# Performance work log

Measured on AMD Instinct MI355X. Metric: run time of the kernel, lower is better.

Reference implementation:

```python
import jax, jax.numpy as jnp
import numpy as np

N, S, D = 512, 64, 128   # num_nodes, seq_len, model_size
H, K = 4, 32             # num_heads, key_size
E = 4096                 # num_edges
WF = 4                   # widening_factor
EPS = 1e-5


def _alibi(num_heads, seq_len):
    slopes = 2.0 ** (-8.0 * (jnp.arange(1, num_heads + 1, dtype=jnp.float32) / num_heads))
    pos = jnp.arange(seq_len, dtype=jnp.float32)
    rel = pos[None, :] - pos[:, None]  # T - t, <= 0 in causal region
    return (slopes[:, None, None] * rel)[None]  # [1,H,S,S]


def layer_norm(x, scale, offset):
    mu = jnp.mean(x, axis=-1, keepdims=True)
    var = jnp.var(x, axis=-1, keepdims=True)
    return (x - mu) * jax.lax.rsqrt(var + EPS) * scale + offset


def segment_softmax(logits, seg, num_segments):
    maxs = jax.ops.segment_max(logits, seg, num_segments=num_segments)
    e = jnp.exp(logits - maxs[seg])
    denom = jax.ops.segment_sum(e, seg, num_segments=num_segments)
    return e / denom[seg]


def setup_inputs() -> dict:
    key = jax.random.key(0)
    ks = jax.random.split(key, 24)
    sd = 0.02
    inp = {
        'nodes': jax.random.normal(ks[0], (N, S, D), jnp.float32),
        'senders': jax.random.randint(ks[1], (E,), 0, N, jnp.int32),
        'receivers': jax.random.randint(ks[2], (E,), 0, N, jnp.int32),
        'alibi_mask': _alibi(H, S),
        'ln1_s': jnp.ones((D,)), 'ln1_b': jnp.zeros((D,)),
        'wq': jax.random.normal(ks[3], (D, H * K)) * sd, 'bq': jnp.zeros((H * K,)),
        'wk': jax.random.normal(ks[4], (D, H * K)) * sd, 'bk': jnp.zeros((H * K,)),
        'wv': jax.random.normal(ks[5], (D, H * K)) * sd, 'bv': jnp.zeros((H * K,)),
        'wo': jax.random.normal(ks[6], (H * K, D)) * sd, 'bo': jnp.zeros((D,)),
        'ln2_s': jnp.ones((D,)), 'ln2_b': jnp.zeros((D,)),
        'w1': jax.random.normal(ks[7], (D, WF * D)) * sd, 'b1': jnp.zeros((WF * D,)),
        'w2': jax.random.normal(ks[8], (WF * D, D)) * sd, 'b2': jnp.zeros((D,)),
        'ln3_s': jnp.ones((D,)), 'ln3_b': jnp.zeros((D,)),
        'w_sa': jax.random.normal(ks[9], (2 * D, D)) * sd, 'b_sa': jnp.zeros((D,)),
        'w_sq': jax.random.normal(ks[10], (D, H * D)) * sd, 'b_sq': jnp.zeros((H * D,)),
    }
    return inp


def reference(nodes, senders, receivers, alibi_mask,
              ln1_s, ln1_b, wq, bq, wk, bk, wv, bv, wo, bo,
              ln2_s, ln2_b, w1, b1, w2, b2, ln3_s, ln3_b,
              w_sa, b_sa, w_sq, b_sq):
    n, s, d = nodes.shape
    # --- node self-attention with ALiBi + causal mask ---
    xn = layer_norm(nodes, ln1_s, ln1_b)
    q = (xn @ wq + bq).reshape(n, s, H, K)
    k = (xn @ wk + bk).reshape(n, s, H, K)
    v = (xn @ wv + bv).reshape(n, s, H, K)
    logits = jnp.einsum('nthk,nThk->nhtT', q, k)
    logits = alibi_mask + logits / jnp.sqrt(jnp.float32(K))
    causal = jnp.tril(jnp.ones((1, 1, s, s), dtype=bool))
    logits = jnp.where(causal, logits, -1e30)
    w = jax.nn.softmax(logits, axis=-1)
    attn = jnp.einsum('nhtT,nThk->nthk', w, v).reshape(n, s, H * K)
    nodes = nodes + (attn @ wo + bo)  # dropout rate 0 (eval)
    # --- FFN block ---
    xn = layer_norm(nodes, ln2_s, ln2_b)
    dense = jax.nn.gelu(xn @ w1 + b1) @ w2 + b2
    nodes = layer_norm(nodes + dense, ln3_s, ln3_b)
    # --- graph message passing: gather / segment-softmax / segment-sum ---
    sent = nodes[senders]        # [E,S,D]
    recv = nodes[receivers]      # [E,S,D]
    sl = jnp.concatenate([sent, recv], axis=-1) @ w_sa + b_sa  # [E,S,D]
    aw = segment_softmax(sl, receivers, n)                     # [E,S,D]
    sq = (aw @ w_sq + b_sq).reshape(E, s, H, d)                # [E,S,H,D]
    messages = jnp.mean(sq * sent[:, :, None, :], axis=2)      # [E,S,D]
    out = jax.ops.segment_sum(messages, receivers, num_segments=n)
    return out
```

## Files before the change

### kernel.cpp

```cpp
#include <hip/hip_runtime.h>
#include <hip/hip_bf16.h>

typedef __hip_bfloat16 bf16;
typedef __attribute__((ext_vector_type(8))) __bf16 bf8v;
typedef __attribute__((ext_vector_type(4))) float  f4v;

#define NN 512
#define SSEQ 64
#define DDIM 128
#define HH 4
#define NROWS (NN*SSEQ)
#define EMAX 4096
#define ECH 64

__device__ __forceinline__ float b2f(bf16 x){ return __bfloat162float(x); }
__device__ __forceinline__ bf16 f2b(float x){ return __float2bfloat16(x); }
__device__ __forceinline__ float ldf(float x){ return x; }
__device__ __forceinline__ float ldf(bf16 x){ return b2f(x); }
__device__ __forceinline__ void stf(float* p, float v){ *p = v; }
__device__ __forceinline__ void stf(bf16* p, float v){ *p = f2b(v); }

__device__ __forceinline__ f4v mfma16(bf8v a, bf8v b, f4v c){
  return __builtin_amdgcn_mfma_f32_16x16x32_bf16(a, b, c, 0, 0, 0);
}
__device__ __forceinline__ bf8v ldfrag(const void* p){
  return __builtin_bit_cast(bf8v, *(const int4*)p);
}

__global__ __launch_bounds__(256) void prep_all_k(
    const float* wq, const float* wk, const float* wv, const float* wo,
    const float* w1, const float* w2, const float* wsa,
    const float* w_sq, const float* b_sq,
    const float* bq, const float* bk, const float* bv,
    bf16* wqkvT, bf16* woT, bf16* w1T, bf16* w2T, bf16* wsaTt,
    bf16* wbarT, float* bbar, float* qkv_bias){
  int b = blockIdx.x, t = threadIdx.x;
  if (b < 832){
    const float* W; bf16* Wt; int K, lN, rel, roff = 0;
    if      (b < 64) { W=wq;  Wt=wqkvT; K=128; lN=7; rel=b;     roff=0;   }
    else if (b <128) { W=wk;  Wt=wqkvT; K=128; lN=7; rel=b-64;  roff=128; }
    else if (b <192) { W=wv;  Wt=wqkvT; K=128; lN=7; rel=b-128; roff=256; }
    else if (b <256) { W=wo;  Wt=woT;   K=128; lN=7; rel=b-192; }
    else if (b <512) { W=w1;  Wt=w1T;   K=128; lN=9; rel=b-256; }
    else if (b <768) { W=w2;  Wt=w2T;   K=512; lN=7; rel=b-512; }
    else             { W=wsa; Wt=wsaTt; K=128; lN=7; rel=b-768; }
    int i = rel*256 + t;
    int k = i >> lN, n = i & ((1<<lN)-1);
    Wt[(size_t)(n+roff)*K + k] = f2b(W[i]);
  } else if (b < 896){
    int i = (b-832)*256 + t;
    int c = i>>7, d = i&127;
    float s = 0.f;
    #pragma unroll
    for (int h=0;h<HH;++h) s += w_sq[(size_t)c*(HH*DDIM) + h*DDIM + d];
    wbarT[d*DDIM + c] = f2b(0.25f*s);
  } else {
    int idx = (b-896)*256 + t;
    if (idx < 128){
      float s = 0.f;
      #pragma unroll
      for (int h=0;h<HH;++h) s += b_sq[h*DDIM + idx];
      bbar[idx] = 0.25f*s;
    } else if (idx < 512){
      int j = idx - 128;
      float v = (j<128) ? bq[j] : (j<256) ? bk[j-128] : bv[j-256];
      qkv_bias[j] = v;
    }
  }
}

__global__ __launch_bounds__(512) void csr_off_k(const int* __restrict__ receivers,
    int* __restrict__ off, int* __restrict__ perm, int E){
  __shared__ int s_cnt[NN];
  int t = threadIdx.x;
  s_cnt[t] = 0;
  __syncthreads();
  for (int e=t; e<E; e+=512) atomicAdd(&s_cnt[receivers[e]], 1);
  __syncthreads();
  int deg = s_cnt[t];
  int acc = 0, myrank = 0;
  for (int i=0;i<NN;++i){
    int di = s_cnt[i];
    acc    += (i<t) ? di : 0;
    myrank += ((di > deg) || (di == deg && i < t)) ? 1 : 0;
  }
  off[t] = acc;
  if (t==NN-1) off[NN] = acc + deg;
  perm[myrank] = t;
}

__global__ __launch_bounds__(64) void hist_k(const int* __restrict__ receivers,
    int* __restrict__ chunk_cnt, int E){
  __shared__ int hc[NN];
  int t = threadIdx.x, c = blockIdx.x;
  for (int i=t;i<NN;i+=64) hc[i]=0;
  __syncthreads();
  int e = c*ECH + t;
  if (e < E) atomicAdd(&hc[receivers[e]], 1);
  __syncthreads();
  for (int i=t;i<NN;i+=64) chunk_cnt[(size_t)c*NN + i] = hc[i];
}

__global__ __launch_bounds__(512) void base_k(const int* __restrict__ off,
    const int* __restrict__ chunk_cnt, int* __restrict__ base, int nch){
  int n = threadIdx.x;
  int run = off[n];
  for (int c=0;c<nch;++c){
    base[(size_t)c*NN + n] = run;
    run += chunk_cnt[(size_t)c*NN + n];
  }
}

__global__ __launch_bounds__(64) void slot_k(const int* __restrict__ senders,
    const int* __restrict__ receivers, const int* __restrict__ base,
    int* __restrict__ slot_snd, int E){
  int t = threadIdx.x, c = blockIdx.x;
  int e = c*ECH + t;
  bool valid = (e < E);
  int r  = valid ? receivers[e] : -1;
  int sd = valid ? senders[e]   : 0;
  int rank = 0;
  #pragma unroll
  for (int i=0;i<64;++i){
    int ri = __shfl(r, i);
    rank += (i < t && ri == r) ? 1 : 0;
  }
  if (valid) slot_snd[base[(size_t)c*NN + r] + rank] = sd;
}

template<typename TIN, typename TOUT>
__global__ __launch_bounds__(256) void ln_k(const TIN* __restrict__ x,
    const float* __restrict__ sc, const float* __restrict__ of,
    TOUT* __restrict__ y){
  int row  = blockIdx.x*4 + (threadIdx.x>>6);
  int lane = threadIdx.x & 63;
  size_t base = (size_t)row*DDIM;
  float v0 = ldf(x[base+lane]);
  float v1 = ldf(x[base+lane+64]);
  float s = v0+v1, q = v0*v0+v1*v1;
  #pragma unroll
  for (int m=1;m<64;m<<=1){ s += __shfl_xor(s,m); q += __shfl_xor(q,m); }
  float mu   = s*(1.0f/DDIM);
  float var  = q*(1.0f/DDIM) - mu*mu;
  float rstd = rsqrtf(var + 1e-5f);
  stf(&y[base+lane],    (v0-mu)*rstd*sc[lane]    + of[lane]);
  stf(&y[base+lane+64], (v1-mu)*rstd*sc[lane+64] + of[lane+64]);
}

template<int KT, int ACT, typename TR, bool RES, bool BIAS>
__global__ __launch_bounds__(256) void gemm_m(const bf16* __restrict__ A,
    const bf16* __restrict__ Wt, const float* __restrict__ bias,
    const TR* __restrict__ R, bf16* __restrict__ C, int N){
  __shared__ bf16 sA[64][72];
  __shared__ bf16 sB[64][72];
  int t = threadIdx.x;
  int bm = blockIdx.x, bn = blockIdx.y;
  int w = t>>6, lane = t&63;
  int wr = w>>1, wc = w&1;
  f4v acc[2][2] = {};
  for (int ks=0; ks<KT; ks+=64){
    #pragma unroll
    for (int p=0;p<2;++p){
      int r = p*32 + (t>>3), cc = (t&7)*8;
      *(int4*)(&sA[r][cc]) = *(const int4*)(A  + (size_t)(bm*64+r)*KT + ks + cc);
      *(int4*)(&sB[r][cc]) = *(const int4*)(Wt + (size_t)(bn*64+r)*KT + ks + cc);
    }
    __syncthreads();
    #pragma unroll
    for (int k0=0;k0<64;k0+=32){
      int kc = k0 + 8*(lane>>4);
      bf8v a0 = ldfrag(&sA[wr*32      + (lane&15)][kc]);
      bf8v a1 = ldfrag(&sA[wr*32 + 16 + (lane&15)][kc]);
      bf8v b0 = ldfrag(&sB[wc*32      + (lane&15)][kc]);
      bf8v b1 = ldfrag(&sB[wc*32 + 16 + (lane&15)][kc]);
      acc[0][0] = mfma16(a0, b0, acc[0][0]);
      acc[0][1] = mfma16(a0, b1, acc[0][1]);
      acc[1][0] = mfma16(a1, b0, acc[1][0]);
      acc[1][1] = mfma16(a1, b1, acc[1][1]);
    }
    __syncthreads();
  }
  #pragma unroll
  for (int j=0;j<2;++j){
    int gcol = bn*64 + wc*32 + j*16 + (lane&15);
    float bs = BIAS ? bias[gcol] : 0.f;
    #pragma unroll
    for (int i=0;i<2;++i){
      #pragma unroll
      for (int r=0;r<4;++r){
        int grow = bm*64 + wr*32 + i*16 + 4*(lane>>4) + r;
        float v = acc[i][j][r] + bs;
        if (ACT==1){
          float xx = v;
          v = 0.5f*xx*(1.0f + tanhf(0.7978845608028654f*(xx + 0.044715f*xx*xx*xx)));
        }
        if (ACT==2) v = __expf(v);
        if (RES) v += ldf(R[(size_t)grow*N + gcol]);
        C[(size_t)grow*N + gcol] = f2b(v);
      }
    }
  }
}

__global__ __launch_bounds__(256) void gemm_wo_ln2_k(const bf16* __restrict__ A,
    const bf16* __restrict__ Wt, const float* __restrict__ bias,
    const float* __restrict__ Rres, const float* __restrict__ lns,
    const float* __restrict__ lnb, bf16* __restrict__ n2out,
    bf16* __restrict__ xnout){
  __shared__ bf16 sA[64][72];
  __shared__ bf16 sB[128][72];
  __shared__ float s_st[2][2][32][2];
  int t = threadIdx.x, bm = blockIdx.x;
  int w = t>>6, lane = t&63, ls = lane&15, lg = lane>>4;
  int wr = w>>1, wc = w&1;
  f4v acc[2][4] = {};
  for (int ks=0; ks<128; ks+=64){
    #pragma unroll
    for (int p=0;p<2;++p){
      int r = p*32 + (t>>3), cc = (t&7)*8;
      *(int4*)(&sA[r][cc]) = *(const int4*)(A + (size_t)(bm*64+r)*128 + ks + cc);
    }
    #pragma unroll
    for (int p=0;p<4;++p){
      int r = p*32 + (t>>3), cc = (t&7)*8;
      *(int4*)(&sB[r][cc]) = *(const int4*)(Wt + (size_t)r*128 + ks + cc);
    }
    __syncthreads();
    #pragma unroll
    for (int k0=0;k0<64;k0+=32){
      int kc = k0 + 8*lg;
      bf8v a0 = ldfrag(&sA[wr*32      + ls][kc]);
      bf8v a1 = ldfrag(&sA[wr*32 + 16 + ls][kc]);
      #pragma unroll
      for (int j=0;j<4;++j){
        bf8v bj = ldfrag(&sB[wc*64 + j*16 + ls][kc]);
        acc[0][j] = mfma16(a0, bj, acc[0][j]);
        acc[1][j] = mfma16(a1, bj, acc[1][j]);
      }
    }
    __syncthreads();
  }
  float x[2][4][4];
  float psum[2][4], psq[2][4];
  #pragma unroll
  for (int i=0;i<2;++i)
    #pragma unroll
    for (int r=0;r<4;++r){ psum[i][r]=0.f; psq[i][r]=0.f; }
  #pragma unroll
  for (int i=0;i<2;++i){
    #pragma unroll
    for (int j=0;j<4;++j){
      int col = wc*64 + j*16 + ls;
      float bs = bias[col];
      #pragma unroll
      for (int r=0;r<4;++r){
        int row = bm*64 + wr*32 + i*16 + 4*lg + r;
        float v = acc[i][j][r] + bs + Rres[(size_t)row*128 + col];
        x[i][j][r] = v;
        psum[i][r] += v;
        psq[i][r]  += v*v;
        n2out[(size_t)row*128 + col] = f2b(v);
      }
    }
  }
  #pragma unroll
  for (int i=0;i<2;++i)
    #pragma unroll
    for (int r=0;r<4;++r){
      float s_=psum[i][r], q_=psq[i][r];
      s_ += __shfl_xor(s_,1); s_ += __shfl_xor(s_,2);
      s_ += __shfl_xor(s_,4); s_ += __shfl_xor(s_,8);
      q_ += __shfl_xor(q_,1); q_ += __shfl_xor(q_,2);
      q_ += __shfl_xor(q_,4); q_ += __shfl_xor(q_,8);
      if (ls == 0){
        int rl = i*16 + 4*lg + r;
        s_st[wr][wc][rl][0] = s_;
        s_st[wr][wc][rl][1] = q_;
      }
    }
  __syncthreads();
  #pragma unroll
  for (int i=0;i<2;++i){
    #pragma unroll
    for (int r=0;r<4;++r){
      int rl = i*16 + 4*lg + r;
      float s_ = s_st[wr][0][rl][0] + s_st[wr][1][rl][0];
      float q_ = s_st[wr][0][rl][1] + s_st[wr][1][rl][1];
      float mu = s_*(1.0f/DDIM);
      float var = q_*(1.0f/DDIM) - mu*mu;
      float rstd = rsqrtf(var + 1e-5f);
      int row = bm*64 + wr*32 + rl;
      #pragma unroll
      for (int j=0;j<4;++j){
        int col = wc*64 + j*16 + ls;
        xnout[(size_t)row*128 + col] = f2b((x[i][j][r]-mu)*rstd*lns[col] + lnb[col]);
      }
    }
  }
}

__global__ __launch_bounds__(256) void gemm_w2_tail_k(const bf16* __restrict__ A,
    const bf16* __restrict__ Wt, const float* __restrict__ bias,
    const bf16* __restrict__ Rres, const float* __restrict__ lns,
    const float* __restrict__ lnb, const bf16* __restrict__ wsaT,
    bf16* __restrict__ r2out, bf16* __restrict__ yexpout){
  __shared__ bf16 sA[64][72];
  __shared__ bf16 sB[128][72];
  __shared__ bf16 sY[64][136];
  __shared__ float s_st[2][2][32][2];
  int t = threadIdx.x, bm = blockIdx.x;
  int w = t>>6, lane = t&63, ls = lane&15, lg = lane>>4;
  int wr = w>>1, wc = w&1;
  f4v acc[2][4] = {};
  for (int ks=0; ks<512; ks+=64){
    #pragma unroll
    for (int p=0;p<2;++p){
      int r = p*32 + (t>>3), cc = (t&7)*8;
      *(int4*)(&sA[r][cc]) = *(const int4*)(A + (size_t)(bm*64+r)*512 + ks + cc);
    }
    #pragma unroll
    for (int p=0;p<4;++p){
      int r = p*32 + (t>>3), cc = (t&7)*8;
      *(int4*)(&sB[r][cc]) = *(const int4*)(Wt + (size_t)r*512 + ks + cc);
    }
    __syncthreads();
    #pragma unroll
    for (int k0=0;k0<64;k0+=32){
      int kc = k0 + 8*lg;
      bf8v a0 = ldfrag(&sA[wr*32      + ls][kc]);
      bf8v a1 = ldfrag(&sA[wr*32 + 16 + ls][kc]);
      #pragma unroll
      for (int j=0;j<4;++j){
        bf8v bj = ldfrag(&sB[wc*64 + j*16 + ls][kc]);
        acc[0][j] = mfma16(a0, bj, acc[0][j]);
        acc[1][j] = mfma16(a1, bj, acc[1][j]);
      }
    }
    __syncthreads();
  }
  float x[2][4][4];
  float psum[2][4], psq[2][4];
  #pragma unroll
  for (int i=0;i<2;++i)
    #pragma unroll
    for (int r=0;r<4;++r){ psum[i][r]=0.f; psq[i][r]=0.f; }
  #pragma unroll
  for (int i=0;i<2;++i){
    #pragma unroll
    for (int j=0;j<4;++j){
      int col = wc*64 + j*16 + ls;
      float bs = bias[col];
      #pragma unroll
      for (int r=0;r<4;++r){
        int row = bm*64 + wr*32 + i*16 + 4*lg + r;
        float v = acc[i][j][r] + bs + b2f(Rres[(size_t)row*128 + col]);
        x[i][j][r] = v;
        psum[i][r] += v;
        psq[i][r]  += v*v;
      }
    }
  }
  #pragma unroll
  for (int i=0;i<2;++i)
    #pragma unroll
    for (int r=0;r<4;++r){
      float s_=psum[i][r], q_=psq[i][r];
      s_ += __shfl_xor(s_,1); s_ += __shfl_xor(s_,2);
      s_ += __shfl_xor(s_,4); s_ += __shfl_xor(s_,8);
      q_ += __shfl_xor(q_,1); q_ += __shfl_xor(q_,2);
      q_ += __shfl_xor(q_,4); q_ += __shfl_xor(q_,8);
      if (ls == 0){
        int rl = i*16 + 4*lg + r;
        s_st[wr][wc][rl][0] = s_;
        s_st[wr][wc][rl][1] = q_;
      }
    }
  __syncthreads();
  #pragma unroll
  for (int i=0;i<2;++i){
    #pragma unroll
    for (int r=0;r<4;++r){
      int rl = i*16 + 4*lg + r;
      float s_ = s_st[wr][0][rl][0] + s_st[wr][1][rl][0];
      float q_ = s_st[wr][0][rl][1] + s_st[wr][1][rl][1];
      float mu = s_*(1.0f/DDIM);
      float var = q_*(1.0f/DDIM) - mu*mu;
      float rstd = rsqrtf(var + 1e-5f);
      int row = bm*64 + wr*32 + rl;
      #pragma unroll
      for (int j=0;j<4;++j){
        int col = wc*64 + j*16 + ls;
        bf16 yb = f2b((x[i][j][r]-mu)*rstd*lns[col] + lnb[col]);
        r2out[(size_t)row*128 + col] = yb;
        sY[wr*32 + rl][col] = yb;
      }
    }
  }
  __syncthreads();
  f4v acc2[2][4] = {};
  for (int ks2=0; ks2<128; ks2+=64){
    #pragma unroll
    for (int p=0;p<4;++p){
      int r = p*32 + (t>>3), cc = (t&7)*8;
      *(int4*)(&sB[r][cc]) = *(const int4*)(wsaT + (size_t)r*128 + ks2 + cc);
    }
    __syncthreads();
    #pragma unroll
    for (int k0=0;k0<64;k0+=32){
      int kc = k0 + 8*lg;
      bf8v a0 = ldfrag(&sY[wr*32      + ls][ks2 + kc]);
      bf8v a1 = ldfrag(&sY[wr*32 + 16 + ls][ks2 + kc]);
      #pragma unroll
      for (int j=0;j<4;++j){
        bf8v bj = ldfrag(&sB[wc*64 + j*16 + ls][kc]);
        acc2[0][j] = mfma16(a0, bj, acc2[0][j]);
        acc2[1][j] = mfma16(a1, bj, acc2[1][j]);
      }
    }
    __syncthreads();
  }
  #pragma unroll
  for (int i=0;i<2;++i){
    #pragma unroll
    for (int j=0;j<4;++j){
      int col = wc*64 + j*16 + ls;
      #pragma unroll
      for (int r=0;r<4;++r){
        int row = bm*64 + wr*32 + i*16 + 4*lg + r;
        yexpout[(size_t)row*128 + col] = f2b(__expf(acc2[i][j][r]));
      }
    }
  }
}

__global__ __launch_bounds__(256) void attn_m(const bf16* __restrict__ qkvb,
    bf16* __restrict__ ob){
  __shared__ bf16 sVT[128][72];
  __shared__ bf16 sP[4][64][72];
  int t = threadIdx.x, n = blockIdx.x;
  int w = t>>6, lane = t&63, ls = lane&15, lg = lane>>4;
  const bf16* qbase = qkvb + (size_t)n*SSEQ*(3*DDIM);
  bf8v qf[4], kf[4];
  #pragma unroll
  for (int mi=0;mi<4;++mi)
    qf[mi] = ldfrag(qbase + (size_t)(16*mi + ls)*(3*DDIM) + 32*w + 8*lg);
  #pragma unroll
  for (int ni=0;ni<4;++ni)
    kf[ni] = ldfrag(qbase + (size_t)(16*ni + ls)*(3*DDIM) + DDIM + 32*w + 8*lg);
  for (int id = t; id < 1024; id += 256){
    int T = id>>4, c = id&15;
    int4 v = *(const int4*)(qbase + (size_t)T*(3*DDIM) + 2*DDIM + c*8);
    const bf16* pv = (const bf16*)&v;
    #pragma unroll
    for (int j=0;j<8;++j){
      int d = c*8 + j;
      sVT[d][T ^ (((d>>3)&7)<<3)] = pv[j];
    }
  }
  f4v accS[4][4];
  #pragma unroll
  for (int mi=0;mi<4;++mi)
    #pragma unroll
    for (int ni=0;ni<4;++ni){
      f4v z = {};
      accS[mi][ni] = mfma16(qf[mi], kf[ni], z);
    }
  __syncthreads();
  const float scale = 0.17677669529663687f;
  const float slope = 1.0f / (float)(4 << (2*w));
  float den[4][4];
  #pragma unroll
  for (int mi=0;mi<4;++mi)
    #pragma unroll
    for (int r=0;r<4;++r) den[mi][r] = 0.f;
  #pragma unroll
  for (int mi=0;mi<4;++mi){
    #pragma unroll
    for (int ni=0;ni<4;++ni){
      #pragma unroll
      for (int r=0;r<4;++r){
        int rel = (16*ni + ls) - (16*mi + 4*lg + r);
        float p = (rel <= 0) ? __expf(accS[mi][ni][r]*scale + slope*(float)rel) : 0.f;
        accS[mi][ni][r] = p;
        den[mi][r] += p;
      }
    }
  }
  #pragma unroll
  for (int mi=0;mi<4;++mi)
    #pragma unroll
    for (int r=0;r<4;++r){
      float d_ = den[mi][r];
      d_ += __shfl_xor(d_, 1);  d_ += __shfl_xor(d_, 2);
      d_ += __shfl_xor(d_, 4);  d_ += __shfl_xor(d_, 8);
      den[mi][r] = 1.0f / d_;
    }
  #pragma unroll
  for (int mi=0;mi<4;++mi)
    #pragma unroll
    for (int ni=0;ni<4;++ni)
      #pragma unroll
      for (int r=0;r<4;++r)
        sP[w][16*mi + 4*lg + r][16*ni + ls] = f2b(accS[mi][ni][r]*den[mi][r]);
  f4v oacc[4][2] = {};
  #pragma unroll
  for (int ks=0;ks<2;++ks){
    bf8v vf[2];
    #pragma unroll
    for (int ni2=0;ni2<2;++ni2){
      int d = 32*w + 16*ni2 + ls;
      vf[ni2] = ldfrag(&sVT[d][(32*ks + 8*lg) ^ (((d>>3)&7)<<3)]);
    }
    #pragma unroll
    for (int mi=0;mi<4;++mi){
      bf8v pa = ldfrag(&sP[w][16*mi + ls][32*ks + 8*lg]);
      #pragma unroll
      for (int ni2=0;ni2<2;++ni2)
        oacc[mi][ni2] = mfma16(pa, vf[ni2], oacc[mi][ni2]);
    }
  }
  #pragma unroll
  for (int mi=0;mi<4;++mi)
    #pragma unroll
    for (int ni2=0;ni2<2;++ni2)
      #pragma unroll
      for (int r=0;r<4;++r)
        ob[(size_t)(n*SSEQ + 16*mi + 4*lg + r)*DDIM + 32*w + 16*ni2 + ls]
          = f2b(oacc[mi][ni2][r]);
}

__global__ __launch_bounds__(128) void msg4_k(const bf16* __restrict__ yexp,
    const bf16* __restrict__ nodes3, const int* __restrict__ off,
    const int* __restrict__ slot_snd, const int* __restrict__ perm,
    const bf16* __restrict__ wbarT, const float* __restrict__ bbar,
    float* __restrict__ out){
  __shared__ bf16  s_sent[2][3][16][72];
  __shared__ float s_den[16][132];
  int t = threadIdx.x, sc = blockIdx.y;
  int n = perm[blockIdx.x];
  int w = t>>6, lane = t&63, ls = lane&15, lg = lane>>4;
  int off0 = off[n], deg = off[n+1]-off0;
  int srow = sc*16 + ls;
  if (deg == 0){
    #pragma unroll
    for (int ct=0;ct<4;++ct)
      #pragma unroll
      for (int r=0;r<4;++r)
        out[((size_t)n*SSEQ + sc*16 + 4*lg + r)*DDIM + w*64 + ct*16 + ls] = 0.f;
    return;
  }
  bf8v B[4][4];
  #pragma unroll
  for (int ct=0;ct<4;++ct)
    #pragma unroll
    for (int kb=0;kb<4;++kb)
      B[ct][kb] = ldfrag(wbarT + (size_t)(w*64 + ct*16 + ls)*DDIM + kb*32 + lg*8);
  float bb[4];
  #pragma unroll
  for (int ct=0;ct<4;++ct) bb[ct] = bbar[w*64 + ct*16 + ls];
  float den[4][8];
  #pragma unroll
  for (int kb=0;kb<4;++kb)
    #pragma unroll
    for (int j=0;j<8;++j) den[kb][j] = 0.f;
  {
    int k = w;
    for (; k+2 < deg; k += 4){
      int s0 = slot_snd[off0+k], s1 = slot_snd[off0+k+2];
      const bf16* y0 = yexp + ((size_t)s0*SSEQ + srow)*DDIM + lg*8;
      const bf16* y1 = yexp + ((size_t)s1*SSEQ + srow)*DDIM + lg*8;
      int4 v0[4], v1[4];
      #pragma unroll
      for (int kb=0;kb<4;++kb) v0[kb] = *(const int4*)(y0 + kb*32);
      #pragma unroll
      for (int kb=0;kb<4;++kb) v1[kb] = *(const int4*)(y1 + kb*32);
      #pragma unroll
      for (int kb=0;kb<4;++kb){
        const bf16* a = (const bf16*)&v0[kb];
        const bf16* b = (const bf16*)&v1[kb];
        #pragma unroll
        for (int j=0;j<8;++j) den[kb][j] += b2f(a[j]) + b2f(b[j]);
      }
    }
    if (k < deg){
      int s0 = slot_snd[off0+k];
      const bf16* y0 = yexp + ((size_t)s0*SSEQ + srow)*DDIM + lg*8;
      #pragma unroll
      for (int kb=0;kb<4;++kb){
        int4 v = *(const int4*)(y0 + kb*32);
        const bf16* a = (const bf16*)&v;
        #pragma unroll
        for (int j=0;j<8;++j) den[kb][j] += b2f(a[j]);
      }
    }
  }
  int l0 = lane*2, l1 = lane*2 + 1;
  int r0 = l0>>3, c0 = (l0&7)*8;
  int r1 = l1>>3, c1 = (l1&7)*8;
  int4 yvA[4], yvB[4], yvC[4];
  {
    int snd = slot_snd[off0];
    const bf16* yr = yexp + ((size_t)snd*SSEQ + srow)*DDIM + lg*8;
    #pragma unroll
    for (int kb=0;kb<4;++kb) yvA[kb] = *(const int4*)(yr + kb*32);
    const bf16* sp = nodes3 + ((size_t)snd*SSEQ + sc*16)*DDIM + w*64;
    *(int4*)&s_sent[w][0][r0][c0] = *(const int4*)(sp + (size_t)r0*DDIM + c0);
    *(int4*)&s_sent[w][0][r1][c1] = *(const int4*)(sp + (size_t)r1*DDIM + c1);
  }
  if (deg > 1){
    int snd = slot_snd[off0+1];
    const bf16* yr = yexp + ((size_t)snd*SSEQ + srow)*DDIM + lg*8;
    #pragma unroll
    for (int kb=0;kb<4;++kb) yvB[kb] = *(const int4*)(yr + kb*32);
    const bf16* sp = nodes3 + ((size_t)snd*SSEQ + sc*16)*DDIM + w*64;
    *(int4*)&s_sent[w][1][r0][c0] = *(const int4*)(sp + (size_t)r0*DDIM + c0);
    *(int4*)&s_sent[w][1][r1][c1] = *(const int4*)(sp + (size_t)r1*DDIM + c1);
  }
  #pragma unroll
  for (int kb=0;kb<4;++kb) yvC[kb] = yvA[kb];
  if (w == 1){
    #pragma unroll
    for (int kb=0;kb<4;++kb)
      #pragma unroll
      for (int j=0;j<8;++j)
        s_den[ls][kb*32 + lg*8 + j] = den[kb][j];
  }
  __syncthreads();
  if (w == 0){
    #pragma unroll
    for (int kb=0;kb<4;++kb)
      #pragma unroll
      for (int j=0;j<8;++j){
        int c = kb*32 + lg*8 + j;
        den[kb][j] = 1.0f / (den[kb][j] + s_den[ls][c]);
        s_den[ls][c] = den[kb][j];
      }
  }
  __syncthreads();
  if (w == 1){
    #pragma unroll
    for (int kb=0;kb<4;++kb)
      #pragma unroll
      for (int j=0;j<8;++j)
        den[kb][j] = s_den[ls][kb*32 + lg*8 + j];
  }
  f4v oacc[4] = {};
  for (int k=0;k<deg;++k){
    if (k+2 < deg){
      int snd2 = slot_snd[off0+k+2];
      const bf16* yr2 = yexp + ((size_t)snd2*SSEQ + srow)*DDIM + lg*8;
      #pragma unroll
      for (int kb=0;kb<4;++kb) yvC[kb] = *(const int4*)(yr2 + kb*32);
      const bf16* sp = nodes3 + ((size_t)snd2*SSEQ + sc*16)*DDIM + w*64;
      int buf2 = (k+2)%3;
      *(int4*)&s_sent[w][buf2][r0][c0] = *(const int4*)(sp + (size_t)r0*DDIM + c0);
      *(int4*)&s_sent[w][buf2][r1][c1] = *(const int4*)(sp + (size_t)r1*DDIM + c1);
    }
    bf8v af[4];
    #pragma unroll
    for (int kb=0;kb<4;++kb){
      const bf16* xv = (const bf16*)&yvA[kb];
      __bf16 tmp[8];
      #pragma unroll
      for (int j=0;j<8;++j){
        bf16 hb_ = f2b(b2f(xv[j]) * den[kb][j]);
        tmp[j] = *(__bf16*)&hb_;
      }
      af[kb] = *(bf8v*)tmp;
    }
    f4v g[4] = {};
    #pragma unroll
    for (int kb=0;kb<4;++kb)
      #pragma unroll
      for (int ct=0;ct<4;++ct)
        g[ct] = mfma16(af[kb], B[ct][kb], g[ct]);
    int buf = k%3;
    #pragma unroll
    for (int ct=0;ct<4;++ct)
      #pragma unroll
      for (int r=0;r<4;++r){
        float sent = b2f(s_sent[w][buf][4*lg + r][ct*16 + ls]);
        oacc[ct][r] += (g[ct][r] + bb[ct]) * sent;
      }
    #pragma unroll
    for (int kb=0;kb<4;++kb){ yvA[kb] = yvB[kb]; yvB[kb] = yvC[kb]; }
  }
  #pragma unroll
  for (int ct=0;ct<4;++ct)
    #pragma unroll
    for (int r=0;r<4;++r)
      out[((size_t)n*SSEQ + sc*16 + 4*lg + r)*DDIM + w*64 + ct*16 + ls] = oacc[ct][r];
}

extern "C" void kernel_launch(void* const* d_in, const int* in_sizes, int n_in,
                              void* d_out, int out_size, void* d_ws, size_t ws_size,
                              hipStream_t stream){
  const float* nodes = (const float*)d_in[0];
  const int*  senders   = (const int*)d_in[1];
  const int*  receivers = (const int*)d_in[2];
  const float* ln1_s=(const float*)d_in[4];  const float* ln1_b=(const float*)d_in[5];
  const float* wq=(const float*)d_in[6];     const float* bq=(const float*)d_in[7];
  const float* wk=(const float*)d_in[8];     const float* bk=(const float*)d_in[9];
  const float* wv=(const float*)d_in[10];    const float* bv_=(const float*)d_in[11];
  const float* wo=(const float*)d_in[12];    const float* bo=(const float*)d_in[13];
  const float* ln2_s=(const float*)d_in[14]; const float* ln2_b=(const float*)d_in[15];
  const float* w1=(const float*)d_in[16];    const float* b1=(const float*)d_in[17];
  const float* w2=(const float*)d_in[18];    const float* b2=(const float*)d_in[19];
  const float* ln3_s=(const float*)d_in[20]; const float* ln3_b=(const float*)d_in[21];
  const float* w_sa=(const float*)d_in[22];
  const float* w_sq=(const float*)d_in[24];  const float* b_sq=(const float*)d_in[25];
  int E = in_sizes[1];
  int nch = (E + ECH - 1)/ECH;

  const size_t MB = 1024*1024;
  char* ws = (char*)d_ws;
  bf16* xn      = (bf16*)(ws);
  bf16* qkvb    = (bf16*)(ws +  8*MB);
  bf16* n2      = (bf16*)(ws + 32*MB);
  bf16* xn2     = (bf16*)(ws + 48*MB);
  bf16* hb      = (bf16*)(ws);
  bf16* attnout = xn;
  bf16* r2     = (bf16*)(ws + 64*MB);
  bf16* yexp   = (bf16*)(ws + 72*MB);
  char* tail = ws + 88*MB;
  bf16*  wbarT   = (bf16*)tail;                       tail += DDIM*DDIM*2;
  float* bbar    = (float*)tail;                      tail += DDIM*4 + 512;
  float* qkv_bias= (float*)tail;                      tail += 3*DDIM*4;
  int*   off     = (int*)tail;                        tail += (NN+8)*4;
  int*   slot_snd= (int*)tail;                        tail += EMAX*4;
  int*   perm    = (int*)tail;                        tail += NN*4;
  int*   ccnt    = (int*)tail;                        tail += 64*NN*4;
  int*   cbase   = (int*)tail;                        tail += 64*NN*4;
  bf16*  wqkvT   = (bf16*)tail;                       tail += 384*128*2;
  bf16*  woT     = (bf16*)tail;                       tail += 128*128*2;
  bf16*  w1T     = (bf16*)tail;                       tail += 128*512*2;
  bf16*  w2T     = (bf16*)tail;                       tail += 512*128*2;
  bf16*  wsaTt   = (bf16*)tail;                       tail += 128*128*2;

  prep_all_k<<<898,256,0,stream>>>(wq,wk,wv,wo,w1,w2,w_sa,w_sq,b_sq,bq,bk,bv_,
                                   wqkvT,woT,w1T,w2T,wsaTt,wbarT,bbar,qkv_bias);
  csr_off_k<<<1,512,0,stream>>>(receivers, off, perm, E);
  hist_k<<<nch,64,0,stream>>>(receivers, ccnt, E);
  base_k<<<1,512,0,stream>>>(off, ccnt, cbase, nch);
  slot_k<<<nch,64,0,stream>>>(senders, receivers, cbase, slot_snd, E);

  ln_k<float,bf16><<<NROWS/4,256,0,stream>>>(nodes, ln1_s, ln1_b, xn);
  gemm_m<128,0,float,false,true><<<dim3(NROWS/64,6),256,0,stream>>>(xn, wqkvT, qkv_bias, (const float*)nullptr, qkvb, 384);
  attn_m<<<NN,256,0,stream>>>(qkvb, attnout);
  gemm_wo_ln2_k<<<NROWS/64,256,0,stream>>>(attnout, woT, bo, nodes, ln2_s, ln2_b, n2, xn2);
  gemm_m<128,1,bf16,false,true><<<dim3(NROWS/64,8),256,0,stream>>>(xn2, w1T, b1, (const bf16*)nullptr, hb, 512);
  gemm_w2_tail_k<<<NROWS/64,256,0,stream>>>(hb, w2T, b2, n2, ln3_s, ln3_b, wsaTt, r2, yexp);

  msg4_k<<<dim3(NN,4),128,0,stream>>>(yexp, r2, off, slot_snd, perm, wbarT, bbar, (float*)d_out);
}
```

Measured before the change: 175.5 us.

## Fuse FFN up-projection with GELU into the down-projection tail kernel

Merges the W1 GEMM+GELU kernel into the W2/LN3/w_sa tail kernel. Each 64-row block computes the full 512-wide hidden activation into shared memory and consumes it directly, so the 32 MB-scale bf16 hidden buffer is never written to or read back from global memory and one launch disappears. The cost is much larger LDS use per block (about 66 KB for sH alone), which lowers occupancy. The W1 phase also runs 8 serial sub-tiles per block with a barrier around each weight load, and grid parallelism drops from 4096 blocks to 512 for that GEMM.

```diff
diff --git a/kernel.cpp b/kernel.cpp
--- a/kernel.cpp
+++ b/kernel.cpp
@@ -25,6 +25,9 @@
 }
 __device__ __forceinline__ bf8v ldfrag(const void* p){
   return __builtin_bit_cast(bf8v, *(const int4*)p);
+}
+__device__ __forceinline__ float gelu_f(float v){
+  return 0.5f*v*(1.0f + tanhf(0.7978845608028654f*(v + 0.044715f*v*v*v)));
 }
 
 __global__ __launch_bounds__(256) void prep_all_k(
@@ -190,10 +193,7 @@
       for (int r=0;r<4;++r){
         int grow = bm*64 + wr*32 + i*16 + 4*(lane>>4) + r;
         float v = acc[i][j][r] + bs;
-        if (ACT==1){
-          float xx = v;
-          v = 0.5f*xx*(1.0f + tanhf(0.7978845608028654f*(xx + 0.044715f*xx*xx*xx)));
-        }
+        if (ACT==1) v = gelu_f(v);
         if (ACT==2) v = __expf(v);
         if (RES) v += ldf(R[(size_t)grow*N + gcol]);
         C[(size_t)grow*N + gcol] = f2b(v);
@@ -299,41 +299,79 @@
   }
 }
 
-__global__ __launch_bounds__(256) void gemm_w2_tail_k(const bf16* __restrict__ A,
-    const bf16* __restrict__ Wt, const float* __restrict__ bias,
-    const bf16* __restrict__ Rres, const float* __restrict__ lns,
+__global__ __launch_bounds__(256) void ffn_k(const bf16* __restrict__ xn2,
+    const bf16* __restrict__ w1T, const float* __restrict__ b1,
+    const bf16* __restrict__ w2T, const float* __restrict__ b2,
+    const bf16* __restrict__ n2res, const float* __restrict__ lns,
     const float* __restrict__ lnb, const bf16* __restrict__ wsaT,
     bf16* __restrict__ r2out, bf16* __restrict__ yexpout){
-  __shared__ bf16 sA[64][72];
-  __shared__ bf16 sB[128][72];
-  __shared__ bf16 sY[64][136];
+  __shared__ bf16 sH[64][520];
+  __shared__ bf16 sW[128*72];
+  __shared__ bf16 sXY[64][136];
   __shared__ float s_st[2][2][32][2];
   int t = threadIdx.x, bm = blockIdx.x;
   int w = t>>6, lane = t&63, ls = lane&15, lg = lane>>4;
   int wr = w>>1, wc = w&1;
-  f4v acc[2][4] = {};
+  #pragma unroll
+  for (int p=0;p<4;++p){
+    int idx = p*256 + t;
+    int r = idx>>4, c8 = (idx&15)*8;
+    *(int4*)(&sXY[r][c8]) = *(const int4*)(xn2 + (size_t)(bm*64+r)*128 + c8);
+  }
+  for (int bn=0; bn<8; ++bn){
+    __syncthreads();
+    #pragma unroll
+    for (int p=0;p<4;++p){
+      int idx = p*256 + t;
+      int r = idx>>4, c8 = (idx&15)*8;
+      *(int4*)(&sW[r*136 + c8]) = *(const int4*)(w1T + (size_t)(bn*64+r)*128 + c8);
+    }
+    __syncthreads();
+    f4v acc[2][2] = {};
+    #pragma unroll
+    for (int k0=0;k0<128;k0+=32){
+      int kc = k0 + 8*lg;
+      bf8v a0  = ldfrag(&sXY[wr*32      + ls][kc]);
+      bf8v a1  = ldfrag(&sXY[wr*32 + 16 + ls][kc]);
+      bf8v b0f = ldfrag(&sW[(wc*32      + ls)*136 + kc]);
+      bf8v b1f = ldfrag(&sW[(wc*32 + 16 + ls)*136 + kc]);
+      acc[0][0] = mfma16(a0, b0f, acc[0][0]);
+      acc[0][1] = mfma16(a0, b1f, acc[0][1]);
+      acc[1][0] = mfma16(a1, b0f, acc[1][0]);
+      acc[1][1] = mfma16(a1, b1f, acc[1][1]);
+    }
+    #pragma unroll
+    for (int j=0;j<2;++j){
+      int colc = wc*32 + j*16 + ls;
+      float bs = b1[bn*64 + colc];
+      #pragma unroll
+      for (int i=0;i<2;++i)
+        #pragma unroll
+        for (int r=0;r<4;++r){
+          int rowl = wr*32 + i*16 + 4*lg + r;
+          sH[rowl][bn*64 + colc] = f2b(gelu_f(acc[i][j][r] + bs));
+        }
+    }
+  }
+  __syncthreads();
+  f4v acc2[2][4] = {};
   for (int ks=0; ks<512; ks+=64){
-    #pragma unroll
-    for (int p=0;p<2;++p){
-      int r = p*32 + (t>>3), cc = (t&7)*8;
-      *(int4*)(&sA[r][cc]) = *(const int4*)(A + (size_t)(bm*64+r)*512 + ks + cc);
-    }
     #pragma unroll
     for (int p=0;p<4;++p){
       int r = p*32 + (t>>3), cc = (t&7)*8;
-      *(int4*)(&sB[r][cc]) = *(const int4*)(Wt + (size_t)r*512 + ks + cc);
+      *(int4*)(&sW[r*72 + cc]) = *(const int4*)(w2T + (size_t)r*512 + ks + cc);
     }
     __syncthreads();
     #pragma unroll
     for (int k0=0;k0<64;k0+=32){
       int kc = k0 + 8*lg;
-      bf8v a0 = ldfrag(&sA[wr*32      + ls][kc]);
-      bf8v a1 = ldfrag(&sA[wr*32 + 16 + ls][kc]);
+      bf8v a0 = ldfrag(&sH[wr*32      + ls][ks + kc]);
+      bf8v a1 = ldfrag(&sH[wr*32 + 16 + ls][ks + kc]);
       #pragma unroll
       for (int j=0;j<4;++j){
-        bf8v bj = ldfrag(&sB[wc*64 + j*16 + ls][kc]);
-        acc[0][j] = mfma16(a0, bj, acc[0][j]);
-        acc[1][j] = mfma16(a1, bj, acc[1][j]);
+        bf8v bj = ldfrag(&sW[(wc*64 + j*16 + ls)*72 + kc]);
+        acc2[0][j] = mfma16(a0, bj, acc2[0][j]);
+        acc2[1][j] = mfma16(a1, bj, acc2[1][j]);
       }
     }
     __syncthreads();
@@ -349,11 +387,11 @@
     #pragma unroll
     for (int j=0;j<4;++j){
       int col = wc*64 + j*16 + ls;
-      float bs = bias[col];
+      float bs = b2[col];
       #pragma unroll
       for (int r=0;r<4;++r){
         int row = bm*64 + wr*32 + i*16 + 4*lg + r;
-        float v = acc[i][j][r] + bs + b2f(Rres[(size_t)row*128 + col]);
+        float v = acc2[i][j][r] + bs + b2f(n2res[(size_t)row*128 + col]);
         x[i][j][r] = v;
         psum[i][r] += v;
         psq[i][r]  += v*v;
@@ -392,45 +430,44 @@
         int col = wc*64 + j*16 + ls;
         bf16 yb = f2b((x[i][j][r]-mu)*rstd*lns[col] + lnb[col]);
         r2out[(size_t)row*128 + col] = yb;
-        sY[wr*32 + rl][col] = yb;
-      }
-    }
-  }
-  __syncthreads();
-  f4v acc2[2][4] = {};
+        sXY[wr*32 + rl][col] = yb;
+      }
+    }
+  }
+  __syncthreads();
+  f4v acc3[2][4] = {};
   for (int ks2=0; ks2<128; ks2+=64){
     #pragma unroll
     for (int p=0;p<4;++p){
       int r = p*32 + (t>>3), cc = (t&7)*8;
-      *(int4*)(&sB[r][cc]) = *(const int4*)(wsaT + (size_t)r*128 + ks2 + cc);
+      *(int4*)(&sW[r*72 + cc]) = *(const int4*)(wsaT + (size_t)r*128 + ks2 + cc);
     }
     __syncthreads();
     #pragma unroll
     for (int k0=0;k0<64;k0+=32){
       int kc = k0 + 8*lg;
-      bf8v a0 = ldfrag(&sY[wr*32      + ls][ks2 + kc]);
-      bf8v a1 = ldfrag(&sY[wr*32 + 16 + ls][ks2 + kc]);
+      bf8v a0 = ldfrag(&sXY[wr*32      + ls][ks2 + kc]);
+      bf8v a1 = ldfrag(&sXY[wr*32 + 16 + ls][ks2 + kc]);
       #pragma unroll
       for (int j=0;j<4;++j){
-        bf8v bj = ldfrag(&sB[wc*64 + j*16 + ls][kc]);
-        acc2[0][j] = mfma16(a0, bj, acc2[0][j]);
-        acc2[1][j] = mfma16(a1, bj, acc2[1][j]);
-      }
-    }
-    __syncthreads();
-  }
-  #pragma unroll
-  for (int i=0;i<2;++i){
+        bf8v bj = ldfrag(&sW[(wc*64 + j*16 + ls)*72 + kc]);
+        acc3[0][j] = mfma16(a0, bj, acc3[0][j]);
+        acc3[1][j] = mfma16(a1, bj, acc3[1][j]);
+      }
+    }
+    __syncthreads();
+  }
+  #pragma unroll
+  for (int i=0;i<2;++i)
     #pragma unroll
     for (int j=0;j<4;++j){
       int col = wc*64 + j*16 + ls;
       #pragma unroll
       for (int r=0;r<4;++r){
         int row = bm*64 + wr*32 + i*16 + 4*lg + r;
-        yexpout[(size_t)row*128 + col] = f2b(__expf(acc2[i][j][r]));
-      }
-    }
-  }
+        yexpout[(size_t)row*128 + col] = f2b(__expf(acc3[i][j][r]));
+      }
+    }
 }
 
 __global__ __launch_bounds__(256) void attn_m(const bf16* __restrict__ qkvb,
@@ -718,7 +755,6 @@
   bf16* qkvb    = (bf16*)(ws +  8*MB);
   bf16* n2      = (bf16*)(ws + 32*MB);
   bf16* xn2     = (bf16*)(ws + 48*MB);
-  bf16* hb      = (bf16*)(ws);
   bf16* attnout = xn;
   bf16* r2     = (bf16*)(ws + 64*MB);
   bf16* yexp   = (bf16*)(ws + 72*MB);
@@ -748,8 +784,7 @@
   gemm_m<128,0,float,false,true><<<dim3(NROWS/64,6),256,0,stream>>>(xn, wqkvT, qkv_bias, (const float*)nullptr, qkvb, 384);
   attn_m<<<NN,256,0,stream>>>(qkvb, attnout);
   gemm_wo_ln2_k<<<NROWS/64,256,0,stream>>>(attnout, woT, bo, nodes, ln2_s, ln2_b, n2, xn2);
-  gemm_m<128,1,bf16,false,true><<<dim3(NROWS/64,8),256,0,stream>>>(xn2, w1T, b1, (const bf16*)nullptr, hb, 512);
-  gemm_w2_tail_k<<<NROWS/64,256,0,stream>>>(hb, w2T, b2, n2, ln3_s, ln3_b, wsaTt, r2, yexp);
+  ffn_k<<<NROWS/64,256,0,stream>>>(xn2, w1T, b1, w2T, b2, n2, ln3_s, ln3_b, wsaTt, r2, yexp);
 
   msg4_k<<<dim3(NN,4),128,0,stream>>>(yexp, r2, off, slot_snd, perm, wbarT, bbar, (float*)d_out);
 }
```

Result: slower. 194.8 us (+11.0%).
